# Kernel optimization log

Measured on AMD Instinct MI355X. Metric: run time of the kernel, lower is better.

## Reference

```python
import jax, jax.numpy as jnp
import numpy as np

N, E, L = 8192, 256, 4  # nodes, emb_dim, relation layers


def setup_inputs() -> dict:
    key = jax.random.key(0)
    k1, k2, k3 = jax.random.split(key, 3)
    emb_ls = jax.random.normal(k1, (N, E), dtype=jnp.float32)
    A_list = jax.random.uniform(k2, (L, N, N), dtype=jnp.float32)
    w = jax.random.normal(k3, (1, 2 * E), dtype=jnp.float32)
    return {"emb_ls": emb_ls, "A_list": A_list, "id": 1000, "w": w}


def reference(emb_ls, A_list, id, w):
    # emb_ls: (N, E), A_list: (L, N, N), w: (1, 2E) -> ans: (1, N)
    n, e = emb_ls.shape
    a_row = A_list[:, id, :]                 # (L, N) adjacency rows for node `id`
    mask = a_row.sum(axis=0) != 0            # neighbors (torch nonzero -> mask, jit-safe)
    # concat[j] = [emb_ls[j], emb_ls[id]]; r = relu(w @ concat.T)
    # split the dot to avoid materializing the (N, 2E) concat:
    w1, w2 = w[0, :e], w[0, e:]
    r = jax.nn.relu(emb_ls @ w1 + jnp.dot(emb_ls[id], w2))  # (N,)
    vals = jnp.sum(a_row * r[None, :], axis=0)               # (N,) weighted scatter-sum
    return jnp.where(mask, vals, jnp.float32(0.0))[None, :]  # (1, N)
```

## Files before the change

### kernel.cpp

```cpp
#include <hip/hip_runtime.h>

#define NN 8192
#define EE 256
#define LL 4

__global__ __launch_bounds__(256) void GraphFilter_kernel(
    const float* __restrict__ emb,
    const float* __restrict__ A,
    const int*   __restrict__ idp,
    const float* __restrict__ w,
    float* __restrict__ out)
{
    const int id   = idp[0];
    const int lane = threadIdx.x & 63;
    const int wave = threadIdx.x >> 6;
    const int j    = blockIdx.x * 4 + wave;

    const int e4 = lane * 4;
    const float4 w1 = *reinterpret_cast<const float4*>(w + e4);
    const float4 w2 = *reinterpret_cast<const float4*>(w + EE + e4);
    const float4 ei = *reinterpret_cast<const float4*>(emb + (size_t)id * EE + e4);
    const float4 er = *reinterpret_cast<const float4*>(emb + (size_t)j  * EE + e4);

    float s = ei.x * w2.x + ei.y * w2.y + ei.z * w2.z + ei.w * w2.w;
    float d = er.x * w1.x + er.y * w1.y + er.z * w1.z + er.w * w1.w;

    #pragma unroll
    for (int off = 32; off >= 1; off >>= 1) {
        s += __shfl_xor(s, off, 64);
        d += __shfl_xor(d, off, 64);
    }

    if (lane == 0) {
        float r = d + s;
        r = r > 0.0f ? r : 0.0f;
        const size_t base = (size_t)id * NN + j;
        const float a0 = A[base];
        const float a1 = A[base + (size_t)1 * NN * NN];
        const float a2 = A[base + (size_t)2 * NN * NN];
        const float a3 = A[base + (size_t)3 * NN * NN];
        const float asum = ((a0 + a1) + a2) + a3;
        out[j] = (asum != 0.0f) ? asum * r : 0.0f;
    }
}

extern "C" void kernel_launch(void* const* d_in, const int* in_sizes, int n_in,
                              void* d_out, int out_size, void* d_ws, size_t ws_size,
                              hipStream_t stream) {
    const float* emb = (const float*)d_in[0];
    const float* A   = (const float*)d_in[1];
    const int*   idp = (const int*)d_in[2];
    const float* w   = (const float*)d_in[3];
    float* out = (float*)d_out;

    dim3 grid(NN / 4);
    dim3 block(256);
    GraphFilter_kernel<<<grid, block, 0, stream>>>(emb, A, idp, w, out);
}
```

Measured before the change: 9.953 us.

## Process eight output rows per wave and hoist adjacency loads before reductions

Each wave now computes eight consecutive outputs instead of one, so the grid shrinks eightfold and the per-wave loads of w and emb[id] are shared across eight rows. The adjacency values are loaded up front as wave-uniform (scalar-addressable) reads and summed early, so their latency overlaps the embedding loads. Results are written with two float4 stores. Fewer blocks (256) may reduce latency hiding across the GPU, and the longer shuffle chain adds per-wave work.

```diff
diff --git a/kernel.cpp b/kernel.cpp
--- a/kernel.cpp
+++ b/kernel.cpp
@@ -3,6 +3,7 @@
 #define NN 8192
 #define EE 256
 #define LL 4
+#define ROWS 8
 
 __global__ __launch_bounds__(256) void GraphFilter_kernel(
     const float* __restrict__ emb,
@@ -13,34 +14,53 @@
 {
     const int id   = idp[0];
     const int lane = threadIdx.x & 63;
-    const int wave = threadIdx.x >> 6;
-    const int j    = blockIdx.x * 4 + wave;
+    const int wv   = __builtin_amdgcn_readfirstlane((int)(threadIdx.x >> 6));
+    const int j0   = (blockIdx.x * 4 + wv) * ROWS;
+
+    float asum[ROWS];
+    #pragma unroll
+    for (int r = 0; r < ROWS; ++r) asum[r] = 0.f;
+    #pragma unroll
+    for (int l = 0; l < LL; ++l) {
+        const float* Ap = A + (size_t)l * NN * NN + (size_t)id * NN + j0;
+        #pragma unroll
+        for (int r = 0; r < ROWS; ++r) asum[r] += Ap[r];
+    }
 
     const int e4 = lane * 4;
     const float4 w1 = *reinterpret_cast<const float4*>(w + e4);
     const float4 w2 = *reinterpret_cast<const float4*>(w + EE + e4);
     const float4 ei = *reinterpret_cast<const float4*>(emb + (size_t)id * EE + e4);
-    const float4 er = *reinterpret_cast<const float4*>(emb + (size_t)j  * EE + e4);
+
+    float4 er[ROWS];
+    #pragma unroll
+    for (int r = 0; r < ROWS; ++r)
+        er[r] = *reinterpret_cast<const float4*>(emb + (size_t)(j0 + r) * EE + e4);
 
     float s = ei.x * w2.x + ei.y * w2.y + ei.z * w2.z + ei.w * w2.w;
-    float d = er.x * w1.x + er.y * w1.y + er.z * w1.z + er.w * w1.w;
+    float d[ROWS];
+    #pragma unroll
+    for (int r = 0; r < ROWS; ++r)
+        d[r] = er[r].x * w1.x + er[r].y * w1.y + er[r].z * w1.z + er[r].w * w1.w;
 
     #pragma unroll
     for (int off = 32; off >= 1; off >>= 1) {
         s += __shfl_xor(s, off, 64);
-        d += __shfl_xor(d, off, 64);
+        #pragma unroll
+        for (int r = 0; r < ROWS; ++r) d[r] += __shfl_xor(d[r], off, 64);
     }
 
     if (lane == 0) {
-        float r = d + s;
-        r = r > 0.0f ? r : 0.0f;
-        const size_t base = (size_t)id * NN + j;
-        const float a0 = A[base];
-        const float a1 = A[base + (size_t)1 * NN * NN];
-        const float a2 = A[base + (size_t)2 * NN * NN];
-        const float a3 = A[base + (size_t)3 * NN * NN];
-        const float asum = ((a0 + a1) + a2) + a3;
-        out[j] = (asum != 0.0f) ? asum * r : 0.0f;
+        float o[ROWS];
+        #pragma unroll
+        for (int r = 0; r < ROWS; ++r) {
+            const float rr = fmaxf(d[r] + s, 0.f);
+            o[r] = (asum[r] != 0.0f) ? asum[r] * rr : 0.0f;
+        }
+        float4 o0 = {o[0], o[1], o[2], o[3]};
+        float4 o1 = {o[4], o[5], o[6], o[7]};
+        *reinterpret_cast<float4*>(out + j0)     = o0;
+        *reinterpret_cast<float4*>(out + j0 + 4) = o1;
     }
 }
 
@@ -53,7 +73,7 @@
     const float* w   = (const float*)d_in[3];
     float* out = (float*)d_out;
 
-    dim3 grid(NN / 4);
+    dim3 grid(NN / (4 * ROWS));
     dim3 block(256);
     GraphFilter_kernel<<<grid, block, 0, stream>>>(emb, A, idp, w, out);
 }
```

Measured after the change: 9.424 us. 1.06x faster.
